# Performance work log

Measured on AMD Instinct MI355X. Metric: run time of the kernel, lower is better.

Reference implementation:

```python
import jax, jax.numpy as jnp
import numpy as np

EPS = 1e-8
AMPLI = 0.0


def setup_inputs() -> dict:
    key = jax.random.key(0)
    k1, k2, k3, k4 = jax.random.split(key, 4)
    B, D, R, O = 8192, 256, 64, 256
    x = jax.random.normal(k1, (B, D), dtype=jnp.float32)
    mu = jax.random.normal(k2, (D, R), dtype=jnp.float32) * 0.1
    sig = jnp.ones((D, R), dtype=jnp.float32)
    W = jax.random.normal(k3, (R, D, O), dtype=jnp.float32) * (1.0 / np.sqrt(D))
    b = jax.random.normal(k4, (R, O), dtype=jnp.float32) * 0.01
    return {"x": x, "mu": mu, "sig": sig, "W": W, "b": b}


def reference(x, mu, sig, W, b):
    # Gaussian membership: frs[b,r] = exp(sum_i -(x[b,i]-mu[i,r])^2 / (2 sig[i,r]^2) + ampli)
    diff = x[:, :, None] - mu[None, :, :]                    # [B, D, R]
    logits = jnp.sum(-(diff ** 2) / (2.0 * sig ** 2), axis=1) + AMPLI  # [B, R]
    frs = jnp.exp(logits)
    # defuzzy: normalize over rules
    f = frs / (jnp.sum(frs, axis=1, keepdims=True) + EPS)    # [B, R]
    # fused weighted sum of per-rule linear experts:
    # out[b,o] = sum_r f[b,r] * (x[b,:] @ W[r] + b[r])
    out = jnp.einsum('br,bi,rio->bo', f, x, W) + f @ b       # [B, O]
    return out
```

## Files before the change

kernel.cpp:

```cpp
#include <hip/hip_runtime.h>
#include <math.h>


constexpr int Bn = 8192, Dn = 256, Rn = 64, On = 256;
constexpr int BROWS = 16;
constexpr int CH = 64;
constexpr float EPS = 1e-8f;
constexpr float SKIP_T = 1e-10f;

__global__ __launch_bounds__(256, 2) void anfis_all(
    const float* __restrict__ x, const float* __restrict__ mu,
    const float* __restrict__ sig, const float* __restrict__ W,
    const float* __restrict__ bb, float* __restrict__ out)
{
  __shared__ float qp[CH * Rn * 2];
  __shared__ float xs[BROWS][68];
  __shared__ float sred[16 * Rn];
  __shared__ int rowflag[BROWS];
  __shared__ int anyflag;

  const int tid = threadIdx.x;
  const int lane = tid & 63;
  const int wv = tid >> 6;
  const int row0 = blockIdx.x * BROWS;
  const int ig = tid >> 4;
  const int rq = (tid & 15) << 2;

  if (tid < BROWS) rowflag[tid] = 0;
  if (tid == 0) anyflag = 0;

  float acc[4] = {0.f, 0.f, 0.f, 0.f};
  float4 sacc = {0.f, 0.f, 0.f, 0.f};

  for (int c = 0; c < 4; ++c) {
    const int i0 = c * CH;
    {
      int r = tid >> 4, c4 = (tid & 15) << 2;
      float4 v = *reinterpret_cast<const float4*>(&x[(size_t)(row0 + r) * Dn + i0 + c4]);
      *reinterpret_cast<float4*>(&xs[r][c4]) = v;
    }
#pragma unroll
    for (int k = 0; k < 4; ++k) {
      int i = ig + k * 16;
      float4 m  = *reinterpret_cast<const float4*>(&mu [(size_t)(i0 + i) * Rn + rq]);
      float4 sg = *reinterpret_cast<const float4*>(&sig[(size_t)(i0 + i) * Rn + rq]);
      float p0 = 0.5f / (sg.x * sg.x), p1 = 0.5f / (sg.y * sg.y);
      float p2 = 0.5f / (sg.z * sg.z), p3 = 0.5f / (sg.w * sg.w);
      float q0 = 2.f * m.x * p0, q1 = 2.f * m.y * p1;
      float q2 = 2.f * m.z * p2, q3 = 2.f * m.w * p3;
      sacc.x = fmaf(m.x * m.x, p0, sacc.x);
      sacc.y = fmaf(m.y * m.y, p1, sacc.y);
      sacc.z = fmaf(m.z * m.z, p2, sacc.z);
      sacc.w = fmaf(m.w * m.w, p3, sacc.w);
      float* dst = &qp[i * 128 + rq * 2];
      *reinterpret_cast<float4*>(dst)     = make_float4(q0, p0, q1, p1);
      *reinterpret_cast<float4*>(dst + 4) = make_float4(q2, p2, q3, p3);
    }
    __syncthreads();
#pragma unroll 4
    for (int i = 0; i < CH; i += 4) {
      float2 a0 = *reinterpret_cast<const float2*>(&qp[(i + 0) * 128 + lane * 2]);
      float2 a1 = *reinterpret_cast<const float2*>(&qp[(i + 1) * 128 + lane * 2]);
      float2 a2 = *reinterpret_cast<const float2*>(&qp[(i + 2) * 128 + lane * 2]);
      float2 a3 = *reinterpret_cast<const float2*>(&qp[(i + 3) * 128 + lane * 2]);
#pragma unroll
      for (int j = 0; j < 4; ++j) {
        float4 xv = *reinterpret_cast<const float4*>(&xs[wv * 4 + j][i]);
        acc[j] = fmaf(xv.x, fmaf(-xv.x, a0.y, a0.x), acc[j]);
        acc[j] = fmaf(xv.y, fmaf(-xv.y, a1.y, a1.x), acc[j]);
        acc[j] = fmaf(xv.z, fmaf(-xv.z, a2.y, a2.x), acc[j]);
        acc[j] = fmaf(xv.w, fmaf(-xv.w, a3.y, a3.x), acc[j]);
      }
    }
    __syncthreads();
  }

  *reinterpret_cast<float4*>(&sred[ig * Rn + rq]) = sacc;
  __syncthreads();
  float Sr = 0.f;
#pragma unroll
  for (int g = 0; g < 16; ++g) Sr += sred[g * Rn + lane];

  float* fb = qp;
#pragma unroll
  for (int j = 0; j < 4; ++j) {
    const int rl = wv * 4 + j, row = row0 + rl;
    float fr = expf(acc[j] - Sr);
    float tot = fr, mx = fr;
#pragma unroll
    for (int m = 1; m < 64; m <<= 1) {
      tot += __shfl_xor(tot, m, 64);
      mx = fmaxf(mx, __shfl_xor(mx, m, 64));
    }
    float inv = 1.f / (tot + EPS);
    float fmax = mx * inv;
    if (fmax < SKIP_T) {
      float4 z = {0.f, 0.f, 0.f, 0.f};
      *reinterpret_cast<float4*>(&out[(size_t)row * On + lane * 4]) = z;
    } else {
      fb[rl * 64 + lane] = fr * inv;
      if (lane == 0) { rowflag[rl] = 1; anyflag = 1; }
    }
  }
  __syncthreads();

  if (anyflag) {
    float* xfull = qp + BROWS * 64;
    for (int rl = 0; rl < BROWS; ++rl) {
      if (!rowflag[rl]) continue;
      const int row = row0 + rl;
      xfull[tid] = x[(size_t)row * Dn + tid];
      __syncthreads();
      float a = 0.f;
      for (int r = 0; r < Rn; ++r) {
        float fr = fb[rl * 64 + r];
        if (fr != 0.f) {
          const float* Wr = &W[((size_t)r * Dn) * On + tid];
          float dot = 0.f;
          for (int i = 0; i < Dn; ++i) dot = fmaf(xfull[i], Wr[(size_t)i * On], dot);
          a = fmaf(fr, dot + bb[(size_t)r * On + tid], a);
        }
      }
      out[(size_t)row * On + tid] = a;
      __syncthreads();
    }
  }
}

extern "C" void kernel_launch(void* const* d_in, const int* in_sizes, int n_in,
                              void* d_out, int out_size, void* d_ws, size_t ws_size,
                              hipStream_t stream) {
  const float* x   = (const float*)d_in[0];
  const float* mu  = (const float*)d_in[1];
  const float* sig = (const float*)d_in[2];
  const float* W   = (const float*)d_in[3];
  const float* b   = (const float*)d_in[4];
  float* out = (float*)d_out;

  anfis_all<<<Bn / BROWS, 256, 0, stream>>>(x, mu, sig, W, b, out);
}
```

Before: 94.67 us.

## Skip per-row rule evaluation using a norm-based upper bound on logits

Drops the full 256x64 membership-logit computation per row. Each row now gets a cheap triangle-inequality bound built from ||x||, per-rule ||mu|| and the minimum 0.5/sig^2: max logit <= -min_p*(|x|-|mu|)^2. Rows whose bound falls below a log threshold are written as zeros, because their normalized firing strengths are provably under the skip threshold. Rows that pass the bound fall back to exact logits, normalization and the expert matmul. The intent is to replace a compute-heavy pass with a memory-bound norm pass, at the cost of extra complexity, and the savings depend on most rows being prunable.

```diff
diff --git a/kernel.cpp b/kernel.cpp
--- a/kernel.cpp
+++ b/kernel.cpp
@@ -3,125 +3,141 @@
 
 
 constexpr int Bn = 8192, Dn = 256, Rn = 64, On = 256;
-constexpr int BROWS = 16;
-constexpr int CH = 64;
+constexpr int BROWS = 32;
 constexpr float EPS = 1e-8f;
 constexpr float SKIP_T = 1e-10f;
+constexpr float LOG_SKIP = -42.0f;
 
-__global__ __launch_bounds__(256, 2) void anfis_all(
+__global__ __launch_bounds__(256) void anfis_fast(
     const float* __restrict__ x, const float* __restrict__ mu,
     const float* __restrict__ sig, const float* __restrict__ W,
     const float* __restrict__ bb, float* __restrict__ out)
 {
-  __shared__ float qp[CH * Rn * 2];
-  __shared__ float xs[BROWS][68];
-  __shared__ float sred[16 * Rn];
-  __shared__ int rowflag[BROWS];
-  __shared__ int anyflag;
+  __shared__ float smin[16 * Rn];
+  __shared__ float ssum[16 * Rn];
+  __shared__ float pminS[Rn];
+  __shared__ float nmuS[Rn];
+  __shared__ int   rowflag[BROWS];
+  __shared__ int   anyflag;
+  __shared__ float xrow[Dn];
+  __shared__ float lred[4 * Rn];
+  __shared__ float fLDS[Rn];
 
   const int tid = threadIdx.x;
-  const int lane = tid & 63;
-  const int wv = tid >> 6;
   const int row0 = blockIdx.x * BROWS;
-  const int ig = tid >> 4;
-  const int rq = (tid & 15) << 2;
 
-  if (tid < BROWS) rowflag[tid] = 0;
+  const int r4 = (tid & 15) << 2;
+  const int ip = tid >> 4;
+  float4 pmin4 = {1e30f, 1e30f, 1e30f, 1e30f};
+  float4 msum4 = {0.f, 0.f, 0.f, 0.f};
+#pragma unroll 4
+  for (int k = 0; k < 16; ++k) {
+    const int i = ip * 16 + k;
+    float4 m = *reinterpret_cast<const float4*>(&mu [(size_t)i * Rn + r4]);
+    float4 s = *reinterpret_cast<const float4*>(&sig[(size_t)i * Rn + r4]);
+    float p0 = 0.5f / (s.x * s.x), p1 = 0.5f / (s.y * s.y);
+    float p2 = 0.5f / (s.z * s.z), p3 = 0.5f / (s.w * s.w);
+    pmin4.x = fminf(pmin4.x, p0); msum4.x = fmaf(m.x, m.x, msum4.x);
+    pmin4.y = fminf(pmin4.y, p1); msum4.y = fmaf(m.y, m.y, msum4.y);
+    pmin4.z = fminf(pmin4.z, p2); msum4.z = fmaf(m.z, m.z, msum4.z);
+    pmin4.w = fminf(pmin4.w, p3); msum4.w = fmaf(m.w, m.w, msum4.w);
+  }
+  *reinterpret_cast<float4*>(&smin[ip * Rn + r4]) = pmin4;
+  *reinterpret_cast<float4*>(&ssum[ip * Rn + r4]) = msum4;
+
+  const int row = tid >> 3;
+  const int sub = tid & 7;
+  const float* xr = x + (size_t)(row0 + row) * Dn + sub * 4;
+  float ss = 0.f;
+#pragma unroll
+  for (int k = 0; k < 8; ++k) {
+    float4 v = *reinterpret_cast<const float4*>(xr + k * 32);
+    ss = fmaf(v.x, v.x, ss); ss = fmaf(v.y, v.y, ss);
+    ss = fmaf(v.z, v.z, ss); ss = fmaf(v.w, v.w, ss);
+  }
+  ss += __shfl_xor(ss, 1); ss += __shfl_xor(ss, 2); ss += __shfl_xor(ss, 4);
+  const float nx = sqrtf(ss);
+
   if (tid == 0) anyflag = 0;
+  __syncthreads();
 
-  float acc[4] = {0.f, 0.f, 0.f, 0.f};
-  float4 sacc = {0.f, 0.f, 0.f, 0.f};
-
-  for (int c = 0; c < 4; ++c) {
-    const int i0 = c * CH;
-    {
-      int r = tid >> 4, c4 = (tid & 15) << 2;
-      float4 v = *reinterpret_cast<const float4*>(&x[(size_t)(row0 + r) * Dn + i0 + c4]);
-      *reinterpret_cast<float4*>(&xs[r][c4]) = v;
+  if (tid < Rn) {
+    float pm = 1e30f, nm = 0.f;
+#pragma unroll
+    for (int g = 0; g < 16; ++g) {
+      pm = fminf(pm, smin[g * Rn + tid]);
+      nm += ssum[g * Rn + tid];
     }
-#pragma unroll
-    for (int k = 0; k < 4; ++k) {
-      int i = ig + k * 16;
-      float4 m  = *reinterpret_cast<const float4*>(&mu [(size_t)(i0 + i) * Rn + rq]);
-      float4 sg = *reinterpret_cast<const float4*>(&sig[(size_t)(i0 + i) * Rn + rq]);
-      float p0 = 0.5f / (sg.x * sg.x), p1 = 0.5f / (sg.y * sg.y);
-      float p2 = 0.5f / (sg.z * sg.z), p3 = 0.5f / (sg.w * sg.w);
-      float q0 = 2.f * m.x * p0, q1 = 2.f * m.y * p1;
-      float q2 = 2.f * m.z * p2, q3 = 2.f * m.w * p3;
-      sacc.x = fmaf(m.x * m.x, p0, sacc.x);
-      sacc.y = fmaf(m.y * m.y, p1, sacc.y);
-      sacc.z = fmaf(m.z * m.z, p2, sacc.z);
-      sacc.w = fmaf(m.w * m.w, p3, sacc.w);
-      float* dst = &qp[i * 128 + rq * 2];
-      *reinterpret_cast<float4*>(dst)     = make_float4(q0, p0, q1, p1);
-      *reinterpret_cast<float4*>(dst + 4) = make_float4(q2, p2, q3, p3);
-    }
-    __syncthreads();
-#pragma unroll 4
-    for (int i = 0; i < CH; i += 4) {
-      float2 a0 = *reinterpret_cast<const float2*>(&qp[(i + 0) * 128 + lane * 2]);
-      float2 a1 = *reinterpret_cast<const float2*>(&qp[(i + 1) * 128 + lane * 2]);
-      float2 a2 = *reinterpret_cast<const float2*>(&qp[(i + 2) * 128 + lane * 2]);
-      float2 a3 = *reinterpret_cast<const float2*>(&qp[(i + 3) * 128 + lane * 2]);
-#pragma unroll
-      for (int j = 0; j < 4; ++j) {
-        float4 xv = *reinterpret_cast<const float4*>(&xs[wv * 4 + j][i]);
-        acc[j] = fmaf(xv.x, fmaf(-xv.x, a0.y, a0.x), acc[j]);
-        acc[j] = fmaf(xv.y, fmaf(-xv.y, a1.y, a1.x), acc[j]);
-        acc[j] = fmaf(xv.z, fmaf(-xv.z, a2.y, a2.x), acc[j]);
-        acc[j] = fmaf(xv.w, fmaf(-xv.w, a3.y, a3.x), acc[j]);
-      }
-    }
-    __syncthreads();
-  }
-
-  *reinterpret_cast<float4*>(&sred[ig * Rn + rq]) = sacc;
-  __syncthreads();
-  float Sr = 0.f;
-#pragma unroll
-  for (int g = 0; g < 16; ++g) Sr += sred[g * Rn + lane];
-
-  float* fb = qp;
-#pragma unroll
-  for (int j = 0; j < 4; ++j) {
-    const int rl = wv * 4 + j, row = row0 + rl;
-    float fr = expf(acc[j] - Sr);
-    float tot = fr, mx = fr;
-#pragma unroll
-    for (int m = 1; m < 64; m <<= 1) {
-      tot += __shfl_xor(tot, m, 64);
-      mx = fmaxf(mx, __shfl_xor(mx, m, 64));
-    }
-    float inv = 1.f / (tot + EPS);
-    float fmax = mx * inv;
-    if (fmax < SKIP_T) {
-      float4 z = {0.f, 0.f, 0.f, 0.f};
-      *reinterpret_cast<float4*>(&out[(size_t)row * On + lane * 4]) = z;
-    } else {
-      fb[rl * 64 + lane] = fr * inv;
-      if (lane == 0) { rowflag[rl] = 1; anyflag = 1; }
-    }
+    pminS[tid] = pm;
+    nmuS[tid] = sqrtf(nm);
   }
   __syncthreads();
 
+  float maxb = -1e30f;
+#pragma unroll
+  for (int rr = 0; rr < 8; ++rr) {
+    const int r = sub * 8 + rr;
+    float d = nx - nmuS[r];
+    maxb = fmaxf(maxb, -pminS[r] * (d * d));
+  }
+  maxb = fmaxf(maxb, __shfl_xor(maxb, 1));
+  maxb = fmaxf(maxb, __shfl_xor(maxb, 2));
+  maxb = fmaxf(maxb, __shfl_xor(maxb, 4));
+  const int flag = (maxb >= LOG_SKIP) ? 1 : 0;
+  if (sub == 0) {
+    rowflag[row] = flag;
+    if (flag) atomicOr(&anyflag, 1);
+  }
+  __syncthreads();
+
+  if (!rowflag[row]) {
+    float4 z = {0.f, 0.f, 0.f, 0.f};
+    float* op = out + (size_t)(row0 + row) * On + sub * 4;
+#pragma unroll
+    for (int k = 0; k < 8; ++k) *reinterpret_cast<float4*>(op + k * 32) = z;
+  }
+
   if (anyflag) {
-    float* xfull = qp + BROWS * 64;
+    const int rl_rule = tid & 63, iq = tid >> 6;
     for (int rl = 0; rl < BROWS; ++rl) {
       if (!rowflag[rl]) continue;
-      const int row = row0 + rl;
-      xfull[tid] = x[(size_t)row * Dn + tid];
+      const int grow = row0 + rl;
+      xrow[tid] = x[(size_t)grow * Dn + tid];
       __syncthreads();
-      float a = 0.f;
-      for (int r = 0; r < Rn; ++r) {
-        float fr = fb[rl * 64 + r];
-        if (fr != 0.f) {
-          const float* Wr = &W[((size_t)r * Dn) * On + tid];
-          float dot = 0.f;
-          for (int i = 0; i < Dn; ++i) dot = fmaf(xfull[i], Wr[(size_t)i * On], dot);
-          a = fmaf(fr, dot + bb[(size_t)r * On + tid], a);
+      float part = 0.f;
+      for (int i = 0; i < 64; ++i) {
+        const int ii = iq * 64 + i;
+        float m = mu [(size_t)ii * Rn + rl_rule];
+        float s = sig[(size_t)ii * Rn + rl_rule];
+        float d = xrow[ii] - m;
+        part = fmaf(d * d, 0.5f / (s * s), part);
+      }
+      lred[iq * Rn + rl_rule] = part;
+      __syncthreads();
+      if (tid < Rn) {
+        float logit = -(lred[tid] + lred[Rn + tid] + lred[2 * Rn + tid] + lred[3 * Rn + tid]);
+        fLDS[tid] = expf(logit);
+      }
+      __syncthreads();
+      float sum = 0.f, mx = 0.f;
+#pragma unroll
+      for (int r = 0; r < Rn; ++r) { sum += fLDS[r]; mx = fmaxf(mx, fLDS[r]); }
+      const float inv = 1.f / (sum + EPS);
+      if (mx * inv < SKIP_T) {
+        out[(size_t)grow * On + tid] = 0.f;
+      } else {
+        float a = 0.f;
+        for (int r = 0; r < Rn; ++r) {
+          float fr = fLDS[r] * inv;
+          if (fr != 0.f) {
+            const float* Wr = &W[((size_t)r * Dn) * On + tid];
+            float dot = 0.f;
+            for (int i = 0; i < Dn; ++i) dot = fmaf(xrow[i], Wr[(size_t)i * On], dot);
+            a = fmaf(fr, dot + bb[(size_t)r * On + tid], a);
+          }
         }
+        out[(size_t)grow * On + tid] = a;
       }
-      out[(size_t)row * On + tid] = a;
       __syncthreads();
     }
   }
@@ -137,5 +153,5 @@
   const float* b   = (const float*)d_in[4];
   float* out = (float*)d_out;
 
-  anfis_all<<<Bn / BROWS, 256, 0, stream>>>(x, mu, sig, W, b, out);
+  anfis_fast<<<Bn / BROWS, 256, 0, stream>>>(x, mu, sig, W, b, out);
 }
```

New measurement: 80.56 us. -14.9%, faster.
